# Kernel optimization log

Measured on AMD Instinct MI355X. Metric: run time of the kernel, lower is better.

Reference implementation:

```python
import jax, jax.numpy as jnp
import numpy as np
import math

B, C, K, P, STRIDE, ITERS = 32, 32, 3, 4, 2, 3
PSIZE = P * P
EPS = 1e-8
LN_2PI = math.log(2.0 * math.pi)


def setup_inputs() -> dict:
    key = jax.random.key(0)
    k1, k2, k3, k4 = jax.random.split(key, 4)
    x = jax.random.uniform(k1, (8, 16, 16, B * (PSIZE + 1)), dtype=jnp.float32)
    weights = jax.random.normal(k2, (1, K * K * B, C, P, P), dtype=jnp.float32)
    beta_u = jax.random.normal(k3, (C,), dtype=jnp.float32) * 0.1
    beta_a = jax.random.normal(k4, (C,), dtype=jnp.float32) * 0.1
    return {"x": x, "weights": weights, "beta_u": beta_u, "beta_a": beta_a}


def _add_patches(x):
    b, h, w, c = x.shape
    oh = ow = (h - K + 1) // STRIDE
    # same nested-list indexing as the torch code: idxs shape [K, oh]
    idxs = np.array([[h_idx + k_idx for h_idx in range(0, h - K + 1, STRIDE)]
                     for k_idx in range(K)])
    x = x[:, idxs, :, :]            # [b, K, oh, w, c]
    x = x[:, :, :, idxs, :]         # [b, K, oh, K, ow, c]
    x = jnp.transpose(x, (0, 1, 3, 2, 4, 5))  # [b, K, K, oh, ow, c]
    return x, oh, ow


def _m_step(a_in, r, v, beta_u, beta_a, inv_temp):
    # v: [n, Bk, C, psize]; a_in: [n, Bk, 1]; r: [n, Bk, C]
    n, Bk, Cc, psize = v.shape
    r = r * a_in
    r = r / (jnp.sum(r, axis=2, keepdims=True) + EPS)
    r_sum = jnp.sum(r, axis=1, keepdims=True)                 # [n,1,C]
    coeff = (r / (r_sum + EPS))[..., None]                    # [n,Bk,C,1]
    mu = jnp.sum(coeff * v, axis=1, keepdims=True)            # [n,1,C,psize]
    sigma_sq = jnp.sum(coeff * (v - mu) ** 2, axis=1, keepdims=True) + EPS
    sig = sigma_sq.reshape(n, Cc, psize)
    cost_h = (beta_u[:, None] + jnp.log(jnp.sqrt(sig))) * r_sum.reshape(n, Cc, 1)
    a_out = jax.nn.sigmoid(inv_temp * (beta_a - jnp.sum(cost_h, axis=2)))  # [n,C]
    return a_out, mu, sigma_sq


def _e_step(mu, sigma_sq, a_out, v):
    ln_p = (-(v - mu) ** 2 / (2.0 * sigma_sq)
            - jnp.log(jnp.sqrt(sigma_sq)) - 0.5 * LN_2PI)     # [n,Bk,C,psize]
    ln_ap = jnp.sum(ln_p, axis=3) + jnp.log(a_out)[:, None, :]
    return jax.nn.softmax(ln_ap, axis=2)


def _em_routing(v, a_in, beta_u, beta_a):
    n, Bk, Cc, psize = v.shape
    r = jnp.full((n, Bk, Cc), 1.0 / Cc, dtype=v.dtype)
    final_lambda = 0.01
    a_out = mu = None
    for it in range(ITERS):  # small fixed loop (3 iters)
        inv_temp = final_lambda * (1.0 - 0.95 ** (it + 1.0))
        a_out, mu, sigma_sq = _m_step(a_in, r, v, beta_u, beta_a, inv_temp)
        if it < ITERS - 1:
            r = _e_step(mu, sigma_sq, a_out, v)
    return mu, a_out


def reference(x, weights, beta_u, beta_a):
    b = x.shape[0]
    xp, oh, ow = _add_patches(x)                 # [b,K,K,oh,ow,544]
    p_in = xp[..., :B * PSIZE].reshape(b * oh * ow, K * K * B, PSIZE)
    a_in = xp[..., B * PSIZE:].reshape(b * oh * ow, K * K * B, 1)
    xv = p_in.reshape(-1, K * K * B, P, P)
    # torch: x.repeat(...,C,1,1) @ w.repeat(b,...) -> batched small matmul
    v = jnp.einsum('nbpq,bcqr->nbcpr', xv, weights[0]).reshape(
        b * oh * ow, K * K * B, C, PSIZE)
    mu, a_out = _em_routing(v, a_in, beta_u, beta_a)
    p_out = mu.reshape(b, oh, ow, C * PSIZE)
    a_o = a_out.reshape(b, oh, ow, C)
    return jnp.concatenate([p_out, a_o], axis=3)  # [b, 7, 7, 544]
```

## Files before the change

kernel.cpp:

```cpp
#include <hip/hip_runtime.h>
#include <math.h>

#define EPS 1e-8f
#define LN_2PI 1.8378770664093453f

#define WS_HALF 827904

__device__ __forceinline__ float redsum32(float v) {
    #pragma unroll
    for (int off = 16; off >= 1; off >>= 1)
        v += __shfl_xor(v, off);
    return v;
}

__device__ __forceinline__ void stage_pixels(const float* __restrict__ x,
                                             float* sbuf, const int n, const int t) {
    for (int idx = t; idx < 9 * 136; idx += 256) {
        const int s  = idx / 136;
        const int e4 = idx - s * 136;
        int cell = n * 9 + s;
        const int b  = cell / 441; cell -= b * 441;
        const int kh = cell / 147; cell -= kh * 147;
        const int kw = cell / 49;  cell -= kw * 49;
        const int i  = cell / 7;
        const int j  = cell - i * 7;
        const float4* src = reinterpret_cast<const float4*>(
            x + (size_t)(((b * 16 + 2 * i + kh) * 16) + 2 * j + kw) * 544);
        reinterpret_cast<float4*>(sbuf + s * 544)[e4] = src[e4];
    }
}

__device__ __forceinline__ void transform_act(float* sbuf, const int t) {
    for (int idx = t; idx < 288; idx += 256) {
        float* ap = sbuf + (idx >> 5) * 544 + 512 + (idx & 31);
        const float a = *ap;
        *ap = a / (a + EPS);
    }
}

__device__ __forceinline__ void compute_v(const float* xp, const float* wp, float* v) {
    float xa[16], wf[16];
    #pragma unroll
    for (int q = 0; q < 4; ++q) {
        float4 tx = reinterpret_cast<const float4*>(xp)[q];
        float4 tw = reinterpret_cast<const float4*>(wp)[q];
        xa[4*q] = tx.x; xa[4*q+1] = tx.y; xa[4*q+2] = tx.z; xa[4*q+3] = tx.w;
        wf[4*q] = tw.x; wf[4*q+1] = tw.y; wf[4*q+2] = tw.z; wf[4*q+3] = tw.w;
    }
    #pragma unroll
    for (int p = 0; p < 4; ++p) {
        #pragma unroll
        for (int r = 0; r < 4; ++r) {
            v[p*4+r] = fmaf(xa[p*4+3], wf[12+r],
                       fmaf(xa[p*4+2], wf[8+r],
                       fmaf(xa[p*4+1], wf[4+r], xa[p*4+0] * wf[r])));
        }
    }
}

__device__ __forceinline__ void publish_partial(float pS0, const float* pS1, const float* pS2,
                                                float red[4][32][36], float* __restrict__ wsb,
                                                const int t, const int c, const int wv) {
    float s0 = pS0 + __shfl_xor(pS0, 32);
    float s1[16], s2[16];
    #pragma unroll
    for (int p = 0; p < 16; ++p) {
        s1[p] = pS1[p] + __shfl_xor(pS1[p], 32);
        s2[p] = pS2[p] + __shfl_xor(pS2[p], 32);
    }
    if ((t & 32) == 0) {
        float* rp = &red[wv][c][0];
        #pragma unroll
        for (int q = 0; q < 4; ++q) {
            reinterpret_cast<float4*>(rp)[q] =
                make_float4(s1[4*q], s1[4*q+1], s1[4*q+2], s1[4*q+3]);
            reinterpret_cast<float4*>(rp + 16)[q] =
                make_float4(s2[4*q], s2[4*q+1], s2[4*q+2], s2[4*q+3]);
        }
        rp[32] = s0;
    }
    __syncthreads();
    const float* rf = &red[0][0][0];
    for (int idx = t; idx < 1056; idx += 256) {
        const int cc = idx / 33;
        const int comp = idx - cc * 33;
        wsb[idx] = rf[(0*32 + cc)*36 + comp] + rf[(1*32 + cc)*36 + comp]
                 + rf[(2*32 + cc)*36 + comp] + rf[(3*32 + cc)*36 + comp];
    }
}

__global__ __launch_bounds__(256, 2)
void caps_it0(const float* __restrict__ x, const float* __restrict__ w,
              float* __restrict__ ws1)
{
    __shared__ __align__(16) float sbuf[9 * 544];
    __shared__ __align__(16) float red[4][32][36];
    const int bid = blockIdx.x;
    const int n = bid >> 1, s = bid & 1;
    const int t = threadIdx.x, c = t & 31, g = t >> 5, wv = t >> 6;

    stage_pixels(x, sbuf, n, t);
    __syncthreads();
    transform_act(sbuf, t);
    __syncthreads();

    float pS0 = 0.0f, pS1[16], pS2[16];
    #pragma unroll
    for (int p = 0; p < 16; ++p) { pS1[p] = 0.0f; pS2[p] = 0.0f; }

    const int hb = s * 8 + g;
    #pragma unroll 1
    for (int k = 0; k < 18; ++k) {
        const int j  = k >> 1;
        const int mi = hb + ((k & 1) << 4);
        float v[16];
        compute_v(sbuf + j * 544 + mi * 16,
                  w + ((size_t)((j << 5) + mi) * 32 + c) * 16, v);
        const float rho = sbuf[j * 544 + 512 + mi] * 0.03125f;
        pS0 += rho;
        #pragma unroll
        for (int p = 0; p < 16; ++p) {
            const float rv = rho * v[p];
            pS1[p] += rv;
            pS2[p] = fmaf(rv, v[p], pS2[p]);
        }
    }
    publish_partial(pS0, pS1, pS2, red, ws1 + (size_t)bid * 1056, t, c, wv);
}

__global__ __launch_bounds__(256, 2)
void caps_estep(const float* __restrict__ x, const float* __restrict__ w,
                const float* __restrict__ bu, const float* __restrict__ ba,
                const float* __restrict__ ws_in, float* __restrict__ ws_out,
                const float itc)
{
    __shared__ __align__(16) float sbuf[9 * 544];
    __shared__ __align__(16) float red[4][32][36];
    float* sred = &red[0][0][0];
    const int bid = blockIdx.x;
    const int n = bid >> 1, s = bid & 1;
    const int t = threadIdx.x, c = t & 31, g = t >> 5, wv = t >> 6;

    stage_pixels(x, sbuf, n, t);
    for (int idx = t; idx < 1056; idx += 256)
        sred[idx] = ws_in[(size_t)(n * 2) * 1056 + idx]
                  + ws_in[(size_t)(n * 2 + 1) * 1056 + idx];
    __syncthreads();
    transform_act(sbuf, t);
    __syncthreads();

    const float* Sc = sred + c * 33;
    const float S0 = Sc[32];
    const float inv = 1.0f / (S0 + EPS);
    float iv[16], dd[16];
    float Cq = 0.0f, shl = 0.0f;
    #pragma unroll
    for (int p = 0; p < 16; ++p) {
        const float S1p = Sc[p], S2p = Sc[16 + p];
        const float m_ = S1p * inv;
        const float sg = (S2p - 2.0f * m_ * S1p + m_ * m_ * S0) * inv + EPS;
        const float ivp = 0.5f / sg;
        iv[p] = ivp;
        dd[p] = -2.0f * m_ * ivp;
        Cq = fmaf(m_ * m_, ivp, Cq);
        shl += 0.5f * __logf(sg);
    }
    const float cost = (16.0f * bu[c] + shl) * S0;
    const float a_out = 1.0f / (1.0f + __expf(-(itc * (ba[c] - cost))));
    const float lapBase = __logf(a_out) - shl - 8.0f * LN_2PI - Cq;
    __syncthreads();

    float pS0 = 0.0f, pS1[16], pS2[16];
    #pragma unroll
    for (int p = 0; p < 16; ++p) { pS1[p] = 0.0f; pS2[p] = 0.0f; }

    const int hb = s * 8 + g;
    #pragma unroll 1
    for (int k = 0; k < 18; ++k) {
        const int j  = k >> 1;
        const int mi = hb + ((k & 1) << 4);
        float v[16];
        compute_v(sbuf + j * 544 + mi * 16,
                  w + ((size_t)((j << 5) + mi) * 32 + c) * 16, v);
        const float f = sbuf[j * 544 + 512 + mi];

        float sA = 0.0f, sB = 0.0f;
        #pragma unroll
        for (int p = 0; p < 16; p += 2) {
            sA = fmaf(fmaf(iv[p],   v[p],   dd[p]),   v[p],   sA);
            sB = fmaf(fmaf(iv[p+1], v[p+1], dd[p+1]), v[p+1], sB);
        }
        const float e = __expf(lapBase - (sA + sB));
        const float z = redsum32(e);
        const float rho = e * __fdividef(f, z);

        pS0 += rho;
        #pragma unroll
        for (int p = 0; p < 16; ++p) {
            const float rv = rho * v[p];
            pS1[p] += rv;
            pS2[p] = fmaf(rv, v[p], pS2[p]);
        }
    }
    publish_partial(pS0, pS1, pS2, red, ws_out + (size_t)bid * 1056, t, c, wv);
}

__global__ __launch_bounds__(256)
void caps_final(const float* __restrict__ ws_in,
                const float* __restrict__ bu, const float* __restrict__ ba,
                float* __restrict__ out)
{
    const int t = threadIdx.x;
    const int n = blockIdx.x * 8 + (t >> 5);
    const int c = t & 31;
    const float* A = ws_in + (size_t)(n * 2) * 1056 + c * 33;
    const float* B = ws_in + (size_t)(n * 2 + 1) * 1056 + c * 33;

    const float S0 = A[32] + B[32];
    const float inv = 1.0f / (S0 + EPS);
    float mu[16], shl = 0.0f;
    #pragma unroll
    for (int p = 0; p < 16; ++p) {
        const float S1p = A[p] + B[p];
        const float S2p = A[16 + p] + B[16 + p];
        const float m_ = S1p * inv;
        const float sg = (S2p - 2.0f * m_ * S1p + m_ * m_ * S0) * inv + EPS;
        mu[p] = m_;
        shl += 0.5f * __logf(sg);
    }
    const float cost = (16.0f * bu[c] + shl) * S0;
    const float a_out = 1.0f / (1.0f + __expf(-(1.42625e-3f * (ba[c] - cost))));

    float* po = out + (size_t)n * 544 + c * 16;
    #pragma unroll
    for (int q = 0; q < 4; ++q) {
        reinterpret_cast<float4*>(po)[q] =
            make_float4(mu[4*q], mu[4*q+1], mu[4*q+2], mu[4*q+3]);
    }
    out[(size_t)n * 544 + 512 + c] = a_out;
}

extern "C" void kernel_launch(void* const* d_in, const int* in_sizes, int n_in,
                              void* d_out, int out_size, void* d_ws, size_t ws_size,
                              hipStream_t stream) {
    const float* x  = (const float*)d_in[0];
    const float* w  = (const float*)d_in[1];
    const float* bu = (const float*)d_in[2];
    const float* ba = (const float*)d_in[3];
    float* out = (float*)d_out;
    float* ws1 = (float*)d_ws;
    float* ws2 = ws1 + WS_HALF;

    caps_it0  <<<784, 256, 0, stream>>>(x, w, ws1);
    caps_estep<<<784, 256, 0, stream>>>(x, w, bu, ba, ws1, ws2, 5.0e-4f);
    caps_estep<<<784, 256, 0, stream>>>(x, w, bu, ba, ws2, ws1, 9.75e-4f);
    caps_final<<<49, 256, 0, stream>>>(ws1, bu, ba, out);
}
```

Before: 87.76 us.

## Fuse EM routing iterations into one cooperative kernel with grid syncs

Merges the four launches (it0, two E-steps, final) into one cooperative kernel that stages and transforms the input pixels into shared memory once and keeps them across iterations, using grid.sync between phases. This removes the repeated input staging and transform and the launch gaps between kernels. It adds three grid-wide barriers, uses a third workspace buffer, and queries device properties and occupancy on every launch. The old multi-kernel path stays as a fallback when the full grid cannot be co-resident.

```diff
diff --git a/kernel.cpp b/kernel.cpp
--- a/kernel.cpp
+++ b/kernel.cpp
@@ -1,10 +1,15 @@
 #include <hip/hip_runtime.h>
+#include <hip/hip_cooperative_groups.h>
 #include <math.h>
+
+namespace cg = cooperative_groups;
 
 #define EPS 1e-8f
 #define LN_2PI 1.8378770664093453f
 
-#define WS_HALF 827904
+#define NBLK 784
+#define WS_STRIDE 1056
+#define WS_BUF (NBLK * WS_STRIDE)
 
 __device__ __forceinline__ float redsum32(float v) {
     #pragma unroll
@@ -89,25 +94,13 @@
     }
 }
 
-__global__ __launch_bounds__(256, 2)
-void caps_it0(const float* __restrict__ x, const float* __restrict__ w,
-              float* __restrict__ ws1)
-{
-    __shared__ __align__(16) float sbuf[9 * 544];
-    __shared__ __align__(16) float red[4][32][36];
-    const int bid = blockIdx.x;
-    const int n = bid >> 1, s = bid & 1;
-    const int t = threadIdx.x, c = t & 31, g = t >> 5, wv = t >> 6;
-
-    stage_pixels(x, sbuf, n, t);
-    __syncthreads();
-    transform_act(sbuf, t);
-    __syncthreads();
-
+__device__ __forceinline__ void it0_phase(const float* sbuf, float red[4][32][36],
+                                          const float* __restrict__ w, float* __restrict__ wsb,
+                                          const int s, const int t, const int c,
+                                          const int g, const int wv) {
     float pS0 = 0.0f, pS1[16], pS2[16];
     #pragma unroll
     for (int p = 0; p < 16; ++p) { pS1[p] = 0.0f; pS2[p] = 0.0f; }
-
     const int hb = s * 8 + g;
     #pragma unroll 1
     for (int k = 0; k < 18; ++k) {
@@ -125,28 +118,21 @@
             pS2[p] = fmaf(rv, v[p], pS2[p]);
         }
     }
-    publish_partial(pS0, pS1, pS2, red, ws1 + (size_t)bid * 1056, t, c, wv);
-}
-
-__global__ __launch_bounds__(256, 2)
-void caps_estep(const float* __restrict__ x, const float* __restrict__ w,
-                const float* __restrict__ bu, const float* __restrict__ ba,
-                const float* __restrict__ ws_in, float* __restrict__ ws_out,
-                const float itc)
-{
-    __shared__ __align__(16) float sbuf[9 * 544];
-    __shared__ __align__(16) float red[4][32][36];
+    publish_partial(pS0, pS1, pS2, red, wsb, t, c, wv);
+}
+
+__device__ __forceinline__ void estep_phase(const float* sbuf, float red[4][32][36],
+                                            const float* __restrict__ w,
+                                            const float* __restrict__ bu,
+                                            const float* __restrict__ ba,
+                                            const float* __restrict__ ws_in,
+                                            float* __restrict__ ws_out, const float itc,
+                                            const int n, const int s, const int t,
+                                            const int c, const int g, const int wv) {
     float* sred = &red[0][0][0];
-    const int bid = blockIdx.x;
-    const int n = bid >> 1, s = bid & 1;
-    const int t = threadIdx.x, c = t & 31, g = t >> 5, wv = t >> 6;
-
-    stage_pixels(x, sbuf, n, t);
     for (int idx = t; idx < 1056; idx += 256)
-        sred[idx] = ws_in[(size_t)(n * 2) * 1056 + idx]
-                  + ws_in[(size_t)(n * 2 + 1) * 1056 + idx];
-    __syncthreads();
-    transform_act(sbuf, t);
+        sred[idx] = ws_in[(size_t)(n * 2) * WS_STRIDE + idx]
+                  + ws_in[(size_t)(n * 2 + 1) * WS_STRIDE + idx];
     __syncthreads();
 
     const float* Sc = sred + c * 33;
@@ -173,7 +159,6 @@
     float pS0 = 0.0f, pS1[16], pS2[16];
     #pragma unroll
     for (int p = 0; p < 16; ++p) { pS1[p] = 0.0f; pS2[p] = 0.0f; }
-
     const int hb = s * 8 + g;
     #pragma unroll 1
     for (int k = 0; k < 18; ++k) {
@@ -183,7 +168,6 @@
         compute_v(sbuf + j * 544 + mi * 16,
                   w + ((size_t)((j << 5) + mi) * 32 + c) * 16, v);
         const float f = sbuf[j * 544 + 512 + mi];
-
         float sA = 0.0f, sB = 0.0f;
         #pragma unroll
         for (int p = 0; p < 16; p += 2) {
@@ -193,7 +177,6 @@
         const float e = __expf(lapBase - (sA + sB));
         const float z = redsum32(e);
         const float rho = e * __fdividef(f, z);
-
         pS0 += rho;
         #pragma unroll
         for (int p = 0; p < 16; ++p) {
@@ -202,7 +185,111 @@
             pS2[p] = fmaf(rv, v[p], pS2[p]);
         }
     }
-    publish_partial(pS0, pS1, pS2, red, ws_out + (size_t)bid * 1056, t, c, wv);
+    publish_partial(pS0, pS1, pS2, red, ws_out, t, c, wv);
+}
+
+__device__ __forceinline__ void final_phase(const float* __restrict__ ws_in,
+                                            const float* __restrict__ bu,
+                                            const float* __restrict__ ba,
+                                            float* __restrict__ out,
+                                            const int n, const int c, const int g) {
+    const float* A = ws_in + (size_t)(n * 2) * WS_STRIDE + c * 33;
+    const float* B = ws_in + (size_t)(n * 2 + 1) * WS_STRIDE + c * 33;
+    const float S0 = A[32] + B[32];
+    const float inv = 1.0f / (S0 + EPS);
+    float mu[16], shl = 0.0f;
+    #pragma unroll
+    for (int p = 0; p < 16; ++p) {
+        const float S1p = A[p] + B[p];
+        const float S2p = A[16 + p] + B[16 + p];
+        const float m_ = S1p * inv;
+        const float sg = (S2p - 2.0f * m_ * S1p + m_ * m_ * S0) * inv + EPS;
+        mu[p] = m_;
+        shl += 0.5f * __logf(sg);
+    }
+    const float cost = (16.0f * bu[c] + shl) * S0;
+    const float a_out = 1.0f / (1.0f + __expf(-(1.42625e-3f * (ba[c] - cost))));
+    if (g == 0) {
+        float* po = out + (size_t)n * 544 + c * 16;
+        #pragma unroll
+        for (int q = 0; q < 4; ++q) {
+            reinterpret_cast<float4*>(po)[q] =
+                make_float4(mu[4*q], mu[4*q+1], mu[4*q+2], mu[4*q+3]);
+        }
+        out[(size_t)n * 544 + 512 + c] = a_out;
+    }
+}
+
+__global__ __launch_bounds__(256, 2)
+void caps_coop(const float* __restrict__ x, const float* __restrict__ w,
+               const float* __restrict__ bu, const float* __restrict__ ba,
+               float* __restrict__ wsA, float* __restrict__ wsB,
+               float* __restrict__ wsC, float* __restrict__ out)
+{
+    cg::grid_group grid = cg::this_grid();
+    __shared__ __align__(16) float sbuf[9 * 544];
+    __shared__ __align__(16) float red[4][32][36];
+
+    const int bid = blockIdx.x;
+    const int n = bid >> 1, s = bid & 1;
+    const int t = threadIdx.x, c = t & 31, g = t >> 5, wv = t >> 6;
+
+    stage_pixels(x, sbuf, n, t);
+    __syncthreads();
+    transform_act(sbuf, t);
+    __syncthreads();
+
+    it0_phase(sbuf, red, w, wsA + (size_t)bid * WS_STRIDE, s, t, c, g, wv);
+    __threadfence();
+    grid.sync();
+
+    estep_phase(sbuf, red, w, bu, ba, wsA, wsB + (size_t)bid * WS_STRIDE,
+                5.0e-4f, n, s, t, c, g, wv);
+    __threadfence();
+    grid.sync();
+
+    estep_phase(sbuf, red, w, bu, ba, wsB, wsC + (size_t)bid * WS_STRIDE,
+                9.75e-4f, n, s, t, c, g, wv);
+    __threadfence();
+    grid.sync();
+
+    if (s == 0)
+        final_phase(wsC, bu, ba, out, n, c, g);
+}
+
+__global__ __launch_bounds__(256, 2)
+void caps_it0(const float* __restrict__ x, const float* __restrict__ w,
+              float* __restrict__ ws1)
+{
+    __shared__ __align__(16) float sbuf[9 * 544];
+    __shared__ __align__(16) float red[4][32][36];
+    const int bid = blockIdx.x;
+    const int n = bid >> 1, s = bid & 1;
+    const int t = threadIdx.x, c = t & 31, g = t >> 5, wv = t >> 6;
+    stage_pixels(x, sbuf, n, t);
+    __syncthreads();
+    transform_act(sbuf, t);
+    __syncthreads();
+    it0_phase(sbuf, red, w, ws1 + (size_t)bid * WS_STRIDE, s, t, c, g, wv);
+}
+
+__global__ __launch_bounds__(256, 2)
+void caps_estep(const float* __restrict__ x, const float* __restrict__ w,
+                const float* __restrict__ bu, const float* __restrict__ ba,
+                const float* __restrict__ ws_in, float* __restrict__ ws_out,
+                const float itc)
+{
+    __shared__ __align__(16) float sbuf[9 * 544];
+    __shared__ __align__(16) float red[4][32][36];
+    const int bid = blockIdx.x;
+    const int n = bid >> 1, s = bid & 1;
+    const int t = threadIdx.x, c = t & 31, g = t >> 5, wv = t >> 6;
+    stage_pixels(x, sbuf, n, t);
+    __syncthreads();
+    transform_act(sbuf, t);
+    __syncthreads();
+    estep_phase(sbuf, red, w, bu, ba, ws_in, ws_out + (size_t)bid * WS_STRIDE,
+                itc, n, s, t, c, g, wv);
 }
 
 __global__ __launch_bounds__(256)
@@ -213,31 +300,7 @@
     const int t = threadIdx.x;
     const int n = blockIdx.x * 8 + (t >> 5);
     const int c = t & 31;
-    const float* A = ws_in + (size_t)(n * 2) * 1056 + c * 33;
-    const float* B = ws_in + (size_t)(n * 2 + 1) * 1056 + c * 33;
-
-    const float S0 = A[32] + B[32];
-    const float inv = 1.0f / (S0 + EPS);
-    float mu[16], shl = 0.0f;
-    #pragma unroll
-    for (int p = 0; p < 16; ++p) {
-        const float S1p = A[p] + B[p];
-        const float S2p = A[16 + p] + B[16 + p];
-        const float m_ = S1p * inv;
-        const float sg = (S2p - 2.0f * m_ * S1p + m_ * m_ * S0) * inv + EPS;
-        mu[p] = m_;
-        shl += 0.5f * __logf(sg);
-    }
-    const float cost = (16.0f * bu[c] + shl) * S0;
-    const float a_out = 1.0f / (1.0f + __expf(-(1.42625e-3f * (ba[c] - cost))));
-
-    float* po = out + (size_t)n * 544 + c * 16;
-    #pragma unroll
-    for (int q = 0; q < 4; ++q) {
-        reinterpret_cast<float4*>(po)[q] =
-            make_float4(mu[4*q], mu[4*q+1], mu[4*q+2], mu[4*q+3]);
-    }
-    out[(size_t)n * 544 + 512 + c] = a_out;
+    final_phase(ws_in, bu, ba, out, n, c, 0);
 }
 
 extern "C" void kernel_launch(void* const* d_in, const int* in_sizes, int n_in,
@@ -248,11 +311,29 @@
     const float* bu = (const float*)d_in[2];
     const float* ba = (const float*)d_in[3];
     float* out = (float*)d_out;
-    float* ws1 = (float*)d_ws;
-    float* ws2 = ws1 + WS_HALF;
-
-    caps_it0  <<<784, 256, 0, stream>>>(x, w, ws1);
-    caps_estep<<<784, 256, 0, stream>>>(x, w, bu, ba, ws1, ws2, 5.0e-4f);
-    caps_estep<<<784, 256, 0, stream>>>(x, w, bu, ba, ws2, ws1, 9.75e-4f);
-    caps_final<<<49, 256, 0, stream>>>(ws1, bu, ba, out);
-}
+    float* wsA = (float*)d_ws;
+    float* wsB = wsA + WS_BUF;
+    float* wsC = wsB + WS_BUF;
+
+    int dev = 0;
+    hipGetDevice(&dev);
+    hipDeviceProp_t prop;
+    hipGetDeviceProperties(&prop, dev);
+    int maxBlocksPerCU = 0;
+    hipOccupancyMaxActiveBlocksPerMultiprocessor(&maxBlocksPerCU,
+                                                 (const void*)caps_coop, 256, 0);
+    const bool coop_ok = (maxBlocksPerCU * prop.multiProcessorCount >= NBLK) &&
+                         prop.cooperativeLaunch;
+
+    if (coop_ok) {
+        void* args[] = {(void*)&x, (void*)&w, (void*)&bu, (void*)&ba,
+                        (void*)&wsA, (void*)&wsB, (void*)&wsC, (void*)&out};
+        hipLaunchCooperativeKernel((const void*)caps_coop, dim3(NBLK), dim3(256),
+                                   args, 0, stream);
+    } else {
+        caps_it0  <<<NBLK, 256, 0, stream>>>(x, w, wsA);
+        caps_estep<<<NBLK, 256, 0, stream>>>(x, w, bu, ba, wsA, wsB, 5.0e-4f);
+        caps_estep<<<NBLK, 256, 0, stream>>>(x, w, bu, ba, wsB, wsC, 9.75e-4f);
+        caps_final<<<49, 256, 0, stream>>>(wsC, bu, ba, out);
+    }
+}
```

New measurement: 86.49 us. No clear change (-1.5%).
